# Kernel tuning notes

Measured on AMD Instinct MI355X. Metric: run time of the kernel, lower is better.

## Reference

```python
import jax, jax.numpy as jnp
import numpy as np

K = 3
SIGMA = 1.0


def setup_inputs() -> dict:
    key = jax.random.key(0)
    k1, k2 = jax.random.split(key)
    B, N = 32, 1024
    predictions = jax.random.normal(k1, (B, N), dtype=jnp.float32)
    # integer relevance grades 0..4, stored as float as in the torch module
    relevance_scores = jax.random.randint(k2, (B, N), 0, 5).astype(jnp.float32)
    return {"predictions": predictions, "relevance_scores": relevance_scores}


def reference(predictions, relevance_scores):
    B, N = predictions.shape
    dt = predictions.dtype

    # lambda weights: rows and columns of top-k predicted items get doubled.
    # weight[b,i,j] = 2^{m[b,i]} * 2^{m[b,j]} with m the top-k membership mask
    _, topk_idx = jax.lax.top_k(predictions, K)  # [B, K]
    m = jnp.zeros((B, N), dtype=dt).at[jnp.arange(B)[:, None], topk_idx].set(1.0)
    mult = 1.0 + m  # 2^m for m in {0,1}
    lambda_weights = mult[:, :, None] * mult[:, None, :]  # [B, N, N]

    pred_diff = predictions[:, :, None] - predictions[:, None, :]  # [B, N, N]
    rel_diff = relevance_scores[:, :, None] - relevance_scores[:, None, :]

    targets = (rel_diff > 0).astype(dt)
    x = SIGMA * pred_diff
    # BCE-with-logits: softplus(x) - t*x  (numerically stable)
    pairwise_loss = jax.nn.softplus(x) - targets * x

    valid_pairs = (rel_diff != 0).astype(dt)
    weighted = pairwise_loss * lambda_weights * valid_pairs
    num_valid = valid_pairs.sum(axis=(1, 2)) + 1e-8
    loss = weighted.sum(axis=(1, 2)) / num_valid
    return loss.mean()
```

## Files before the change

### kernel.cpp

```cpp
#include <hip/hip_runtime.h>
#include <math.h>

#define NN 1024
#define BTH 256
#define NT 16
#define NTILES 136
#define TBLK 34

__device__ __forceinline__ float pair_f(float pi, float ri, float pj, float rj) {
    const float x = pi - pj;
    const float y = (ri > rj) ? -x : x;
    const float e = __expf(-fabsf(y));
    const float f = fmaxf(y, 0.0f) + __logf(1.0f + e);
    return (ri != rj) ? f : 0.0f;
}

__global__ void __launch_bounds__(BTH)
main_kernel(const float* __restrict__ pred, const float* __restrict__ rel,
            float* __restrict__ psum, float* __restrict__ corr,
            float* __restrict__ cntv, int B) {
    const int t = threadIdx.x;
    const int blk = blockIdx.x;
    const int ntb = TBLK * B;

    if (blk < ntb) {
        __shared__ float2 s_seg[4][64];
        const int w = t >> 6, l = t & 63;
        const int b = blk / TBLK;
        const int L = (blk % TBLK) * 4 + w;
        int rem = L, ti = 0;
        while (rem >= NT - ti) { rem -= NT - ti; ++ti; }
        const int tj = ti + rem;
        const size_t base = (size_t)b * NN;
        const int i0 = ti * 64, j0 = tj * 64;

        const float jp = pred[base + j0 + l];
        const float jr = rel [base + j0 + l];
        s_seg[w][l] = make_float2(pred[base + i0 + l], rel[base + i0 + l]);

        float acc = 0.0f;
        if (ti != tj) {
#pragma unroll 16
            for (int ii = 0; ii < 64; ++ii) {
                const float2 v = s_seg[w][ii];
                acc += pair_f(v.x, v.y, jp, jr);
            }
        } else {
#pragma unroll 16
            for (int ii = 0; ii < 64; ++ii) {
                const float2 v = s_seg[w][ii];
                const float f = pair_f(v.x, v.y, jp, jr);
                acc += (l > ii) ? f : 0.0f;
            }
        }
        for (int off = 32; off > 0; off >>= 1) acc += __shfl_down(acc, off);
        if (l == 0) psum[(size_t)b * NTILES + L] = acc * 2.0f;
    } else {
        const int b = blk - ntb;
        __shared__ float s_p[NN];
        __shared__ float s_r[NN];
        __shared__ float s_wk[NN];
        __shared__ float s_val[BTH];
        __shared__ int   s_idx[BTH];
        __shared__ int   s_win[3];
        __shared__ int   s_hist[5];
        __shared__ float s_red[4];
        const size_t base = (size_t)b * NN;

        if (t < 5) s_hist[t] = 0;
        __syncthreads();
        const float4 p4 = ((const float4*)(pred + base))[t];
        const float4 r4 = ((const float4*)(rel  + base))[t];
        ((float4*)s_p)[t]  = p4;
        ((float4*)s_r)[t]  = r4;
        ((float4*)s_wk)[t] = p4;
        atomicAdd(&s_hist[(int)r4.x], 1);
        atomicAdd(&s_hist[(int)r4.y], 1);
        atomicAdd(&s_hist[(int)r4.z], 1);
        atomicAdd(&s_hist[(int)r4.w], 1);
        __syncthreads();

        for (int k = 0; k < 3; ++k) {
            float bv = -INFINITY; int bi = NN;
            for (int n = t; n < NN; n += BTH) {
                const float v = s_wk[n];
                if (v > bv) { bv = v; bi = n; }
            }
            s_val[t] = bv; s_idx[t] = bi;
            __syncthreads();
            for (int off = BTH / 2; off > 0; off >>= 1) {
                if (t < off) {
                    const float ov = s_val[t + off]; const int oi = s_idx[t + off];
                    if (ov > s_val[t] || (ov == s_val[t] && oi < s_idx[t])) {
                        s_val[t] = ov; s_idx[t] = oi;
                    }
                }
                __syncthreads();
            }
            if (t == 0) { s_win[k] = s_idx[0]; s_wk[s_idx[0]] = -INFINITY; }
            __syncthreads();
        }

        float part = 0.0f;
        for (int k = 0; k < 3; ++k) {
            const int row = s_win[k];
            const float pk = s_p[row], rk = s_r[row];
            for (int c = 0; c < 4; ++c) {
                const int j = t + c * BTH;
                part += pair_f(pk, rk, s_p[j], s_r[j]);
            }
        }
        for (int off = 32; off > 0; off >>= 1) part += __shfl_down(part, off);
        if ((t & 63) == 0) s_red[t >> 6] = part;
        __syncthreads();
        if (t == 0) {
            const float R = s_red[0] + s_red[1] + s_red[2] + s_red[3];
            const int a = s_win[0], c2 = s_win[1], d = s_win[2];
            const float TT = 2.0f * (pair_f(s_p[a],  s_r[a],  s_p[c2], s_r[c2])
                                   + pair_f(s_p[a],  s_r[a],  s_p[d],  s_r[d])
                                   + pair_f(s_p[c2], s_r[c2], s_p[d],  s_r[d]));
            corr[b] = 2.0f * R + TT;
            int s2 = 0;
            for (int g = 0; g < 5; ++g) s2 += s_hist[g] * s_hist[g];
            cntv[b] = (float)(NN * NN - s2);
        }
    }
}

__global__ void finalize_kernel(const float* __restrict__ psum,
                                const float* __restrict__ corr,
                                const float* __restrict__ cntv,
                                float* __restrict__ out, int B) {
    const int t = threadIdx.x;
    __shared__ float s_l[32];
    const int b = t >> 3, k = t & 7;
    float s = 0.0f;
    if (b < B) {
        for (int e = k; e < NTILES; e += 8) s += psum[(size_t)b * NTILES + e];
    }
    s += __shfl_xor(s, 1);
    s += __shfl_xor(s, 2);
    s += __shfl_xor(s, 4);
    if (b < B && k == 0) s_l[b] = (s + corr[b]) / (cntv[b] + 1e-8f);
    __syncthreads();
    if (t == 0) {
        float m = 0.0f;
        for (int i = 0; i < B; ++i) m += s_l[i];
        out[0] = m / (float)B;
    }
}

extern "C" void kernel_launch(void* const* d_in, const int* in_sizes, int n_in,
                              void* d_out, int out_size, void* d_ws, size_t ws_size,
                              hipStream_t stream) {
    const float* pred = (const float*)d_in[0];
    const float* rel  = (const float*)d_in[1];
    float* out = (float*)d_out;

    const int B = in_sizes[0] / NN;

    float* psum = (float*)d_ws;
    float* corr = psum + (size_t)B * NTILES;
    float* cntv = corr + B;

    main_kernel<<<TBLK * B + B, BTH, 0, stream>>>(pred, rel, psum, corr, cntv, B);
    finalize_kernel<<<1, BTH, 0, stream>>>(psum, corr, cntv, out, B);
}
```

Baseline: 24.77 us.

## Fuse finalize into main kernel via last-block counter and faster top-k

Merges the finalize kernel into the main kernel: each block increments a global counter, and the block that sees the count reach a multiple of the grid size performs the final reduction. The top-k blocks move to the start of the grid and now use wave ballots for the histogram and register plus shuffle reductions for top-3, replacing shared-memory tree reductions with many barriers. The counter relies on the workspace starting at zero and is never reset, using a modulo check. The pair-tile blocks now declare the larger shared arrays, which may reduce how many blocks fit per CU.

```diff
diff --git a/kernel.cpp b/kernel.cpp
--- a/kernel.cpp
+++ b/kernel.cpp
@@ -16,18 +16,92 @@
 }
 
 __global__ void __launch_bounds__(BTH)
-main_kernel(const float* __restrict__ pred, const float* __restrict__ rel,
-            float* __restrict__ psum, float* __restrict__ corr,
-            float* __restrict__ cntv, int B) {
+fused_kernel(const float* __restrict__ pred, const float* __restrict__ rel,
+             float* __restrict__ psum, float* __restrict__ corr,
+             float* __restrict__ cntv, unsigned int* __restrict__ ctr,
+             float* __restrict__ out, int B) {
     const int t = threadIdx.x;
+    const int w = t >> 6, l = t & 63;
     const int blk = blockIdx.x;
-    const int ntb = TBLK * B;
 
-    if (blk < ntb) {
-        __shared__ float2 s_seg[4][64];
-        const int w = t >> 6, l = t & 63;
-        const int b = blk / TBLK;
-        const int L = (blk % TBLK) * 4 + w;
+    __shared__ float s_p[NN];
+    __shared__ float s_r[NN];
+    __shared__ float s_rv[3][4];
+    __shared__ int   s_ri[3][4];
+    __shared__ int   s_hist[4][5];
+    __shared__ float s_red[4];
+    __shared__ float s_l[32];
+    __shared__ int   s_flag;
+
+    if (blk < B) {
+        const int b = blk;
+        const size_t base = (size_t)b * NN;
+        const float4 p4 = ((const float4*)(pred + base))[t];
+        const float4 r4 = ((const float4*)(rel  + base))[t];
+        ((float4*)s_p)[t] = p4;
+        ((float4*)s_r)[t] = r4;
+
+        for (int g = 0; g < 5; ++g) {
+            const float gf = (float)g;
+            int c = __popcll(__ballot(r4.x == gf)) + __popcll(__ballot(r4.y == gf))
+                  + __popcll(__ballot(r4.z == gf)) + __popcll(__ballot(r4.w == gf));
+            if (l == 0) s_hist[w][g] = c;
+        }
+
+        int w1 = -1, w2 = -1, w3 = -1;
+        const int n0 = t * 4;
+        for (int k = 0; k < 3; ++k) {
+            float bv = -INFINITY;
+            int   bi = NN;
+            if (n0 + 0 != w1 && n0 + 0 != w2 && p4.x > bv) { bv = p4.x; bi = n0 + 0; }
+            if (n0 + 1 != w1 && n0 + 1 != w2 && p4.y > bv) { bv = p4.y; bi = n0 + 1; }
+            if (n0 + 2 != w1 && n0 + 2 != w2 && p4.z > bv) { bv = p4.z; bi = n0 + 2; }
+            if (n0 + 3 != w1 && n0 + 3 != w2 && p4.w > bv) { bv = p4.w; bi = n0 + 3; }
+            for (int off = 32; off > 0; off >>= 1) {
+                const float ov = __shfl_xor(bv, off);
+                const int   oi = __shfl_xor(bi, off);
+                if (ov > bv || (ov == bv && oi < bi)) { bv = ov; bi = oi; }
+            }
+            if (l == 0) { s_rv[k][w] = bv; s_ri[k][w] = bi; }
+            __syncthreads();
+            bv = s_rv[k][0]; bi = s_ri[k][0];
+            for (int q = 1; q < 4; ++q) {
+                const float ov = s_rv[k][q]; const int oi = s_ri[k][q];
+                if (ov > bv || (ov == bv && oi < bi)) { bv = ov; bi = oi; }
+            }
+            if (k == 0) w1 = bi; else if (k == 1) w2 = bi; else w3 = bi;
+        }
+
+        float part = 0.0f;
+        for (int k = 0; k < 3; ++k) {
+            const int row = (k == 0) ? w1 : (k == 1) ? w2 : w3;
+            const float pk = s_p[row], rk = s_r[row];
+#pragma unroll
+            for (int c = 0; c < 4; ++c) {
+                const int j = t + c * BTH;
+                part += pair_f(pk, rk, s_p[j], s_r[j]);
+            }
+        }
+        for (int off = 32; off > 0; off >>= 1) part += __shfl_down(part, off);
+        if (l == 0) s_red[w] = part;
+        __syncthreads();
+        if (t == 0) {
+            const float R = s_red[0] + s_red[1] + s_red[2] + s_red[3];
+            const float TT = 2.0f * (pair_f(s_p[w1], s_r[w1], s_p[w2], s_r[w2])
+                                   + pair_f(s_p[w1], s_r[w1], s_p[w3], s_r[w3])
+                                   + pair_f(s_p[w2], s_r[w2], s_p[w3], s_r[w3]));
+            corr[b] = 2.0f * R + TT;
+            int s2 = 0;
+            for (int g = 0; g < 5; ++g) {
+                const int cg = s_hist[0][g] + s_hist[1][g] + s_hist[2][g] + s_hist[3][g];
+                s2 += cg * cg;
+            }
+            cntv[b] = (float)(NN * NN - s2);
+        }
+    } else {
+        const int idx = blk - B;
+        const int b = idx / TBLK;
+        const int L = (idx % TBLK) * 4 + w;
         int rem = L, ti = 0;
         while (rem >= NT - ti) { rem -= NT - ti; ++ti; }
         const int tj = ti + rem;
@@ -36,117 +110,50 @@
 
         const float jp = pred[base + j0 + l];
         const float jr = rel [base + j0 + l];
-        s_seg[w][l] = make_float2(pred[base + i0 + l], rel[base + i0 + l]);
+        s_p[w * 64 + l] = pred[base + i0 + l];
+        s_r[w * 64 + l] = rel [base + i0 + l];
 
         float acc = 0.0f;
         if (ti != tj) {
 #pragma unroll 16
-            for (int ii = 0; ii < 64; ++ii) {
-                const float2 v = s_seg[w][ii];
-                acc += pair_f(v.x, v.y, jp, jr);
-            }
+            for (int ii = 0; ii < 64; ++ii)
+                acc += pair_f(s_p[w * 64 + ii], s_r[w * 64 + ii], jp, jr);
         } else {
 #pragma unroll 16
             for (int ii = 0; ii < 64; ++ii) {
-                const float2 v = s_seg[w][ii];
-                const float f = pair_f(v.x, v.y, jp, jr);
+                const float f = pair_f(s_p[w * 64 + ii], s_r[w * 64 + ii], jp, jr);
                 acc += (l > ii) ? f : 0.0f;
             }
         }
         for (int off = 32; off > 0; off >>= 1) acc += __shfl_down(acc, off);
         if (l == 0) psum[(size_t)b * NTILES + L] = acc * 2.0f;
-    } else {
-        const int b = blk - ntb;
-        __shared__ float s_p[NN];
-        __shared__ float s_r[NN];
-        __shared__ float s_wk[NN];
-        __shared__ float s_val[BTH];
-        __shared__ int   s_idx[BTH];
-        __shared__ int   s_win[3];
-        __shared__ int   s_hist[5];
-        __shared__ float s_red[4];
-        const size_t base = (size_t)b * NN;
+    }
 
-        if (t < 5) s_hist[t] = 0;
-        __syncthreads();
-        const float4 p4 = ((const float4*)(pred + base))[t];
-        const float4 r4 = ((const float4*)(rel  + base))[t];
-        ((float4*)s_p)[t]  = p4;
-        ((float4*)s_r)[t]  = r4;
-        ((float4*)s_wk)[t] = p4;
-        atomicAdd(&s_hist[(int)r4.x], 1);
-        atomicAdd(&s_hist[(int)r4.y], 1);
-        atomicAdd(&s_hist[(int)r4.z], 1);
-        atomicAdd(&s_hist[(int)r4.w], 1);
-        __syncthreads();
-
-        for (int k = 0; k < 3; ++k) {
-            float bv = -INFINITY; int bi = NN;
-            for (int n = t; n < NN; n += BTH) {
-                const float v = s_wk[n];
-                if (v > bv) { bv = v; bi = n; }
-            }
-            s_val[t] = bv; s_idx[t] = bi;
-            __syncthreads();
-            for (int off = BTH / 2; off > 0; off >>= 1) {
-                if (t < off) {
-                    const float ov = s_val[t + off]; const int oi = s_idx[t + off];
-                    if (ov > s_val[t] || (ov == s_val[t] && oi < s_idx[t])) {
-                        s_val[t] = ov; s_idx[t] = oi;
-                    }
-                }
-                __syncthreads();
-            }
-            if (t == 0) { s_win[k] = s_idx[0]; s_wk[s_idx[0]] = -INFINITY; }
-            __syncthreads();
+    __syncthreads();
+    if (t == 0) {
+        __threadfence();
+        const unsigned int old = atomicAdd(ctr, 1u);
+        s_flag = (((old + 1u) % (unsigned int)gridDim.x) == 0u) ? 1 : 0;
+    }
+    __syncthreads();
+    if (s_flag) {
+        __threadfence();
+        const int bb = t >> 3;
+        const int k  = t & 7;
+        float s = 0.0f;
+        if (bb < B) {
+            for (int e = k; e < NTILES; e += 8) s += psum[(size_t)bb * NTILES + e];
         }
-
-        float part = 0.0f;
-        for (int k = 0; k < 3; ++k) {
-            const int row = s_win[k];
-            const float pk = s_p[row], rk = s_r[row];
-            for (int c = 0; c < 4; ++c) {
-                const int j = t + c * BTH;
-                part += pair_f(pk, rk, s_p[j], s_r[j]);
-            }
-        }
-        for (int off = 32; off > 0; off >>= 1) part += __shfl_down(part, off);
-        if ((t & 63) == 0) s_red[t >> 6] = part;
+        s += __shfl_xor(s, 1);
+        s += __shfl_xor(s, 2);
+        s += __shfl_xor(s, 4);
+        if (bb < B && k == 0) s_l[bb] = (s + corr[bb]) / (cntv[bb] + 1e-8f);
         __syncthreads();
         if (t == 0) {
-            const float R = s_red[0] + s_red[1] + s_red[2] + s_red[3];
-            const int a = s_win[0], c2 = s_win[1], d = s_win[2];
-            const float TT = 2.0f * (pair_f(s_p[a],  s_r[a],  s_p[c2], s_r[c2])
-                                   + pair_f(s_p[a],  s_r[a],  s_p[d],  s_r[d])
-                                   + pair_f(s_p[c2], s_r[c2], s_p[d],  s_r[d]));
-            corr[b] = 2.0f * R + TT;
-            int s2 = 0;
-            for (int g = 0; g < 5; ++g) s2 += s_hist[g] * s_hist[g];
-            cntv[b] = (float)(NN * NN - s2);
+            float m = 0.0f;
+            for (int i = 0; i < B; ++i) m += s_l[i];
+            out[0] = m / (float)B;
         }
-    }
-}
-
-__global__ void finalize_kernel(const float* __restrict__ psum,
-                                const float* __restrict__ corr,
-                                const float* __restrict__ cntv,
-                                float* __restrict__ out, int B) {
-    const int t = threadIdx.x;
-    __shared__ float s_l[32];
-    const int b = t >> 3, k = t & 7;
-    float s = 0.0f;
-    if (b < B) {
-        for (int e = k; e < NTILES; e += 8) s += psum[(size_t)b * NTILES + e];
-    }
-    s += __shfl_xor(s, 1);
-    s += __shfl_xor(s, 2);
-    s += __shfl_xor(s, 4);
-    if (b < B && k == 0) s_l[b] = (s + corr[b]) / (cntv[b] + 1e-8f);
-    __syncthreads();
-    if (t == 0) {
-        float m = 0.0f;
-        for (int i = 0; i < B; ++i) m += s_l[i];
-        out[0] = m / (float)B;
     }
 }
 
@@ -159,10 +166,10 @@
 
     const int B = in_sizes[0] / NN;
 
-    float* psum = (float*)d_ws;
+    unsigned int* ctr = (unsigned int*)d_ws;
+    float* psum = (float*)((char*)d_ws + 64);
     float* corr = psum + (size_t)B * NTILES;
     float* cntv = corr + B;
 
-    main_kernel<<<TBLK * B + B, BTH, 0, stream>>>(pred, rel, psum, corr, cntv, B);
-    finalize_kernel<<<1, BTH, 0, stream>>>(psum, corr, cntv, out, B);
+    fused_kernel<<<B + TBLK * B, BTH, 0, stream>>>(pred, rel, psum, corr, cntv, ctr, out, B);
 }
```

After: 34.16 us. +37.9%, slower.
